# Performance work log

Hardware: AMD Instinct MI355X
Metric: run time of the kernel (lower is better)

The kernel has to match this reference:

```python
import jax, jax.numpy as jnp
import numpy as np

B, C, N, K = 2, 64, 20000, 16
COUT = 64


def setup_inputs() -> dict:
    key = jax.random.key(0)
    k1, k2, k3, k4, k5 = jax.random.split(key, 5)
    x = jax.random.normal(k1, (B, C, N, 1), dtype=jnp.float32)
    edge_index = jax.random.randint(k2, (2, B, N, K), 0, N)
    pos = jax.random.normal(k3, (B, 3, N, 1), dtype=jnp.float32)
    # BasicConv([2C, COUT]) -> 1x1 Conv2d weight [COUT, 2C] (+bias), then ReLU
    W = jax.random.normal(k4, (COUT, 2 * C), dtype=jnp.float32) * (1.0 / np.sqrt(2 * C))
    b = jax.random.normal(k5, (COUT,), dtype=jnp.float32) * 0.01
    return {"x": x, "edge_index": edge_index, "pos": pos, "W": W, "b": b}


def _gather(t, idx):
    # t: [B, C, N, 1], idx: [B, N, K] -> [B, C, N, K]
    t3 = t[..., 0]  # [B, C, N]
    return jax.vmap(lambda tb, ib: tb[:, ib])(t3, idx)


def reference(x, edge_index, pos, W, b):
    x_i = _gather(x, edge_index[1])           # [B, C, N, K] center
    x_j = _gather(x, edge_index[0])           # [B, C, N, K] neighbor
    feat = jnp.concatenate([x_i, x_j - x_i], axis=1)  # [B, 2C, N, K]
    # 1x1 conv + bias + ReLU
    out = jnp.einsum('oc,bcnk->bonk', W, feat) + b[None, :, None, None]
    out = jax.nn.relu(out)
    # distance-based suppression
    pos_i = _gather(pos, edge_index[1])       # [B, 3, N, K]
    pos_j = _gather(pos, edge_index[0])
    dis = jnp.sqrt(jnp.sum(jnp.square(pos_j - pos_i), axis=1))  # [B, N, K]
    suppression = 2.0 * jax.nn.sigmoid(-dis)[:, None, :, :]     # [B, 1, N, K]
    out = out * suppression
    max_value = jnp.max(out, axis=-1, keepdims=True)             # [B, COUT, N, 1]
    return max_value
```

## Files before the change

### kernel.cpp

```cpp
#include <hip/hip_runtime.h>
#include <math.h>

#define B_    2
#define C_    64
#define N_    20000
#define K_    16
#define COUT_ 64
#define TN1   64
#define NB1   ((N_ + TN1 - 1) / TN1)
#define TN2   16
#define NB2   (N_ / TN2)

typedef unsigned int   u32;
typedef unsigned short u16;

static __device__ __forceinline__ u16 f2bf(float f) {
    union { float f; u32 u; } v; v.f = f;
    u32 r = (v.u + 0x7FFFu + ((v.u >> 16) & 1u)) >> 16;
    return (u16)r;
}
static __device__ __forceinline__ float uasf(u32 u) {
    union { u32 u; float f; } v; v.u = u; return v.f;
}

__global__ __launch_bounds__(256)
void stage1(const float* __restrict__ x, const float* __restrict__ W,
            const float* __restrict__ bias,
            u16* __restrict__ zbuf, u16* __restrict__ ybuf) {
    __shared__ float xt[64][68];
    __shared__ float wc[64][130];

    const int bi   = blockIdx.x;
    const int b    = bi / NB1;
    const int n0   = (bi % NB1) * TN1;
    const int t    = threadIdx.x;
    const int lane = t & 63;
    const int w    = t >> 6;

    #pragma unroll
    for (int r = 0; r < 16; ++r) {
        int flat = r * 256 + t;
        int o = flat >> 6, c = flat & 63;
        float w1 = W[o * 128 + c];
        float w2 = W[o * 128 + 64 + c];
        wc[c][2 * o]     = w1 - w2;
        wc[c][2 * o + 1] = w2;
    }
    const float* xb = x + (size_t)b * C_ * N_;
    #pragma unroll
    for (int r = 0; r < 4; ++r) {
        int flat = r * 256 + t;
        int c = flat >> 4, ng = (flat & 15) * 4;
        int n = n0 + ng;
        float4 v;
        if (n + 3 < N_) {
            v = *(const float4*)&xb[c * N_ + n];
        } else {
            v.x = (n     < N_) ? xb[c * N_ + n    ] : 0.0f;
            v.y = (n + 1 < N_) ? xb[c * N_ + n + 1] : 0.0f;
            v.z = (n + 2 < N_) ? xb[c * N_ + n + 2] : 0.0f;
            v.w = (n + 3 < N_) ? xb[c * N_ + n + 3] : 0.0f;
        }
        *(float4*)&xt[c][ng] = v;
    }
    const float bo = bias[lane];
    __syncthreads();

    const int nb = w * 16;
    float4 z0 = {bo,bo,bo,bo}, z1 = z0, z2 = z0, z3 = z0;
    float4 y0 = {0,0,0,0},     y1 = y0, y2 = y0, y3 = y0;

#define FMA4(ZR, YR, XV) \
    ZR.x = fmaf(wv.x, XV.x, ZR.x);  YR.x = fmaf(wv.y, XV.x, YR.x); \
    ZR.y = fmaf(wv.x, XV.y, ZR.y);  YR.y = fmaf(wv.y, XV.y, YR.y); \
    ZR.z = fmaf(wv.x, XV.z, ZR.z);  YR.z = fmaf(wv.y, XV.z, YR.z); \
    ZR.w = fmaf(wv.x, XV.w, ZR.w);  YR.w = fmaf(wv.y, XV.w, YR.w);

    #pragma unroll 2
    for (int c = 0; c < 64; ++c) {
        float2 wv = *(const float2*)&wc[c][2 * lane];
        float4 xa = *(const float4*)&xt[c][nb];
        float4 xv1 = *(const float4*)&xt[c][nb + 4];
        float4 xv2 = *(const float4*)&xt[c][nb + 8];
        float4 xv3 = *(const float4*)&xt[c][nb + 12];
        FMA4(z0, y0, xa)
        FMA4(z1, y1, xv1)
        FMA4(z2, y2, xv2)
        FMA4(z3, y3, xv3)
    }
#undef FMA4

    {
        const size_t rowb = (size_t)b * N_;
        auto st = [&](int i, float zv, float yv) {
            int n = n0 + nb + i;
            if (n < N_) {
                size_t off = (rowb + n) * 64 + lane;
                zbuf[off] = f2bf(zv);
                ybuf[off] = f2bf(yv);
            }
        };
        st(0,  z0.x, y0.x); st(1,  z0.y, y0.y); st(2,  z0.z, y0.z); st(3,  z0.w, y0.w);
        st(4,  z1.x, y1.x); st(5,  z1.y, y1.y); st(6,  z1.z, y1.z); st(7,  z1.w, y1.w);
        st(8,  z2.x, y2.x); st(9,  z2.y, y2.y); st(10, z2.z, y2.z); st(11, z2.w, y2.w);
        st(12, z3.x, y3.x); st(13, z3.y, y3.y); st(14, z3.z, y3.z); st(15, z3.w, y3.w);
    }
}

__global__ __launch_bounds__(256)
void stage2(const int* __restrict__ ei, const float* __restrict__ pos,
            const u16* __restrict__ zbuf, const u16* __restrict__ ybuf,
            float* __restrict__ out) {
    __shared__ uint2 esl[TN2][17];
    __shared__ float tile[TN2][66];

    const int bi   = blockIdx.x;
    const int b    = bi / NB2;
    const int n0   = (bi % NB2) * TN2;
    const int t    = threadIdx.x;
    const int nl   = t >> 4;
    const int kh   = (t >> 3) & 1;
    const int cq   = t & 7;

    {
        const int    idx = n0 * K_ + t;
        const int*   e0  = ei + (size_t)b * N_ * K_;
        const int*   e1  = ei + ((size_t)B_ + b) * N_ * K_;
        const float* pb  = pos + (size_t)b * 3 * N_;
        int i0 = e0[idx], i1 = e1[idx];
        float dx = pb[i0]          - pb[i1];
        float dy = pb[N_ + i0]     - pb[N_ + i1];
        float dz = pb[2 * N_ + i0] - pb[2 * N_ + i1];
        float dis = sqrtf(dx * dx + dy * dy + dz * dz);
        float s = 2.0f / (1.0f + __expf(dis));
        esl[t >> 4][t & 15] = make_uint2((u32)i0 | ((u32)i1 << 16),
                                         __float_as_uint(s));
    }
    __syncthreads();

    const u16* zb = zbuf + (size_t)b * N_ * 64;
    const u16* yb = ybuf + (size_t)b * N_ * 64;

    float4 ma = {0,0,0,0}, mb = {0,0,0,0};

#define COMB(ZW, YW, MLO, MHI) { \
    float zl = uasf((ZW) << 16), zh = uasf((ZW) & 0xFFFF0000u); \
    float yl = uasf((YW) << 16), yh = uasf((YW) & 0xFFFF0000u); \
    MLO = fmaxf(MLO, fmaxf(zl + yl, 0.0f) * s); \
    MHI = fmaxf(MHI, fmaxf(zh + yh, 0.0f) * s); }

    #pragma unroll
    for (int i = 0; i < 8; ++i) {
        int   k = 2 * i + kh;
        uint2 e = esl[nl][k];
        int   i0 = (int)(e.x & 0xFFFFu);
        int   i1 = (int)(e.x >> 16);
        float s  = uasf(e.y);
        uint4 z4 = *((const uint4*)(zb + ((size_t)i1 << 6)) + cq);
        uint4 y4 = *((const uint4*)(yb + ((size_t)i0 << 6)) + cq);
        COMB(z4.x, y4.x, ma.x, ma.y)
        COMB(z4.y, y4.y, ma.z, ma.w)
        COMB(z4.z, y4.z, mb.x, mb.y)
        COMB(z4.w, y4.w, mb.z, mb.w)
    }
#undef COMB

    ma.x = fmaxf(ma.x, __shfl_xor(ma.x, 8));
    ma.y = fmaxf(ma.y, __shfl_xor(ma.y, 8));
    ma.z = fmaxf(ma.z, __shfl_xor(ma.z, 8));
    ma.w = fmaxf(ma.w, __shfl_xor(ma.w, 8));
    mb.x = fmaxf(mb.x, __shfl_xor(mb.x, 8));
    mb.y = fmaxf(mb.y, __shfl_xor(mb.y, 8));
    mb.z = fmaxf(mb.z, __shfl_xor(mb.z, 8));
    mb.w = fmaxf(mb.w, __shfl_xor(mb.w, 8));

    if (kh == 0) {
        int cb = cq * 8;
        *(float2*)&tile[nl][cb]     = make_float2(ma.x, ma.y);
        *(float2*)&tile[nl][cb + 2] = make_float2(ma.z, ma.w);
        *(float2*)&tile[nl][cb + 4] = make_float2(mb.x, mb.y);
        *(float2*)&tile[nl][cb + 6] = make_float2(mb.z, mb.w);
    }
    __syncthreads();

    #pragma unroll
    for (int r = 0; r < 4; ++r) {
        int flat = r * 256 + t;
        int o = flat >> 4, n2 = flat & 15;
        __builtin_nontemporal_store(tile[n2][o],
            &out[((size_t)b * COUT_ + o) * N_ + n0 + n2]);
    }
}

extern "C" void kernel_launch(void* const* d_in, const int* in_sizes, int n_in,
                              void* d_out, int out_size, void* d_ws, size_t ws_size,
                              hipStream_t stream) {
    const float* x    = (const float*)d_in[0];
    const int*   ei   = (const int*)  d_in[1];
    const float* pos  = (const float*)d_in[2];
    const float* W    = (const float*)d_in[3];
    const float* bias = (const float*)d_in[4];
    float*       out  = (float*)d_out;

    const size_t tabElems = (size_t)B_ * N_ * 64;
    u16* zbuf = (u16*)d_ws;
    u16* ybuf = zbuf + tabElems;

    hipLaunchKernelGGL(stage1, dim3(B_ * NB1), dim3(256), 0, stream,
                       x, W, bias, zbuf, ybuf);
    hipLaunchKernelGGL(stage2, dim3(B_ * NB2), dim3(256), 0, stream,
                       ei, pos, zbuf, ybuf, out);
}
```

Measured before the change: 107.9 us.

## Gather bf16 edge features into LDS and run per-edge conv with MFMA

```diff
diff --git a/kernel.cpp b/kernel.cpp
--- a/kernel.cpp
+++ b/kernel.cpp
@@ -6,13 +6,15 @@
 #define N_    20000
 #define K_    16
 #define COUT_ 64
-#define TN1   64
-#define NB1   ((N_ + TN1 - 1) / TN1)
-#define TN2   16
-#define NB2   (N_ / TN2)
+#define TNC   64
+#define NBC   ((N_ + TNC - 1) / TNC)
+#define TN    16
+#define NB    (N_ / TN)
 
 typedef unsigned int   u32;
 typedef unsigned short u16;
+typedef __attribute__((ext_vector_type(8))) short bf16x8;
+typedef __attribute__((ext_vector_type(4))) float f32x4;
 
 static __device__ __forceinline__ u16 f2bf(float f) {
     union { float f; u32 u; } v; v.f = f;
@@ -22,31 +24,43 @@
 static __device__ __forceinline__ float uasf(u32 u) {
     union { u32 u; float f; } v; v.u = u; return v.f;
 }
+static __device__ __forceinline__ u32 bfsub2(u32 bv, u32 av) {
+    float bl = uasf(bv << 16), bh = uasf(bv & 0xFFFF0000u);
+    float al = uasf(av << 16), ah = uasf(av & 0xFFFF0000u);
+    return (u32)f2bf(bl - al) | ((u32)f2bf(bh - ah) << 16);
+}
+
+#define SWZ(row, off) ((off) ^ (((row) & 7) << 4))
 
 __global__ __launch_bounds__(256)
-void stage1(const float* __restrict__ x, const float* __restrict__ W,
-            const float* __restrict__ bias,
-            u16* __restrict__ zbuf, u16* __restrict__ ybuf) {
-    __shared__ float xt[64][68];
-    __shared__ float wc[64][130];
-
-    const int bi   = blockIdx.x;
-    const int b    = bi / NB1;
-    const int n0   = (bi % NB1) * TN1;
-    const int t    = threadIdx.x;
-    const int lane = t & 63;
-    const int w    = t >> 6;
-
-    #pragma unroll
-    for (int r = 0; r < 16; ++r) {
-        int flat = r * 256 + t;
-        int o = flat >> 6, c = flat & 63;
-        float w1 = W[o * 128 + c];
-        float w2 = W[o * 128 + 64 + c];
-        wc[c][2 * o]     = w1 - w2;
-        wc[c][2 * o + 1] = w2;
-    }
-    const float* xb = x + (size_t)b * C_ * N_;
+void precast(const float* __restrict__ x, const float* __restrict__ W,
+             u16* __restrict__ xb, u16* __restrict__ wfrag) {
+    const int bi = blockIdx.x;
+    const int t  = threadIdx.x;
+
+    if (bi == B_ * NBC) {
+        const int l  = t & 63;
+        const int ot = t >> 6;
+        const int ro = (ot * 16 + (l & 15)) * 128 + ((l >> 4) << 3);
+        #pragma unroll
+        for (int ks = 0; ks < 4; ++ks) {
+            u32 p[4];
+            #pragma unroll
+            for (int jj = 0; jj < 4; ++jj) {
+                float v0 = W[ro + ks * 32 + 2 * jj];
+                float v1 = W[ro + ks * 32 + 2 * jj + 1];
+                p[jj] = (u32)f2bf(v0) | ((u32)f2bf(v1) << 16);
+            }
+            *(uint4*)&wfrag[(size_t)((ot * 4 + ks) * 64 + l) * 8] =
+                make_uint4(p[0], p[1], p[2], p[3]);
+        }
+        return;
+    }
+
+    __shared__ float tile[64][68];
+    const int b  = bi / NBC;
+    const int n0 = (bi % NBC) * TNC;
+    const float* xbase = x + (size_t)b * C_ * N_;
     #pragma unroll
     for (int r = 0; r < 4; ++r) {
         int flat = r * 256 + t;
@@ -54,132 +68,141 @@
         int n = n0 + ng;
         float4 v;
         if (n + 3 < N_) {
-            v = *(const float4*)&xb[c * N_ + n];
+            v = *(const float4*)&xbase[c * N_ + n];
         } else {
-            v.x = (n     < N_) ? xb[c * N_ + n    ] : 0.0f;
-            v.y = (n + 1 < N_) ? xb[c * N_ + n + 1] : 0.0f;
-            v.z = (n + 2 < N_) ? xb[c * N_ + n + 2] : 0.0f;
-            v.w = (n + 3 < N_) ? xb[c * N_ + n + 3] : 0.0f;
-        }
-        *(float4*)&xt[c][ng] = v;
-    }
-    const float bo = bias[lane];
-    __syncthreads();
-
-    const int nb = w * 16;
-    float4 z0 = {bo,bo,bo,bo}, z1 = z0, z2 = z0, z3 = z0;
-    float4 y0 = {0,0,0,0},     y1 = y0, y2 = y0, y3 = y0;
-
-#define FMA4(ZR, YR, XV) \
-    ZR.x = fmaf(wv.x, XV.x, ZR.x);  YR.x = fmaf(wv.y, XV.x, YR.x); \
-    ZR.y = fmaf(wv.x, XV.y, ZR.y);  YR.y = fmaf(wv.y, XV.y, YR.y); \
-    ZR.z = fmaf(wv.x, XV.z, ZR.z);  YR.z = fmaf(wv.y, XV.z, YR.z); \
-    ZR.w = fmaf(wv.x, XV.w, ZR.w);  YR.w = fmaf(wv.y, XV.w, YR.w);
-
-    #pragma unroll 2
-    for (int c = 0; c < 64; ++c) {
-        float2 wv = *(const float2*)&wc[c][2 * lane];
-        float4 xa = *(const float4*)&xt[c][nb];
-        float4 xv1 = *(const float4*)&xt[c][nb + 4];
-        float4 xv2 = *(const float4*)&xt[c][nb + 8];
-        float4 xv3 = *(const float4*)&xt[c][nb + 12];
-        FMA4(z0, y0, xa)
-        FMA4(z1, y1, xv1)
-        FMA4(z2, y2, xv2)
-        FMA4(z3, y3, xv3)
-    }
-#undef FMA4
+            v.x = (n     < N_) ? xbase[c * N_ + n    ] : 0.0f;
+            v.y = (n + 1 < N_) ? xbase[c * N_ + n + 1] : 0.0f;
+            v.z = (n + 2 < N_) ? xbase[c * N_ + n + 2] : 0.0f;
+            v.w = (n + 3 < N_) ? xbase[c * N_ + n + 3] : 0.0f;
+        }
+        *(float4*)&tile[c][ng] = v;
+    }
+    __syncthreads();
+
+    const int n = t >> 2, q = t & 3;
+    if (n0 + n < N_) {
+        u32 p[8];
+        #pragma unroll
+        for (int jj = 0; jj < 8; ++jj) {
+            float v0 = tile[q * 16 + 2 * jj][n];
+            float v1 = tile[q * 16 + 2 * jj + 1][n];
+            p[jj] = (u32)f2bf(v0) | ((u32)f2bf(v1) << 16);
+        }
+        u16* dst = xb + ((size_t)(b * N_ + n0 + n)) * 64 + q * 16;
+        *(uint4*)dst       = make_uint4(p[0], p[1], p[2], p[3]);
+        *(uint4*)(dst + 8) = make_uint4(p[4], p[5], p[6], p[7]);
+    }
+}
+
+__global__ __launch_bounds__(256)
+void fused(const int* __restrict__ ei, const float* __restrict__ pos,
+           const u16* __restrict__ xb, const u16* __restrict__ wfrag,
+           const float* __restrict__ bias, float* __restrict__ out) {
+    __shared__ u16   feat[256 * 128];
+    __shared__ uint2 esl[256];
+    __shared__ float otile[16][66];
+
+    const int bi   = blockIdx.x;
+    const int b    = bi / NB;
+    const int n0   = (bi % NB) * TN;
+    const int t    = threadIdx.x;
+    const int lane = t & 63;
+    const int w    = t >> 6;
+    const int g    = lane >> 4;
 
     {
-        const size_t rowb = (size_t)b * N_;
-        auto st = [&](int i, float zv, float yv) {
-            int n = n0 + nb + i;
-            if (n < N_) {
-                size_t off = (rowb + n) * 64 + lane;
-                zbuf[off] = f2bf(zv);
-                ybuf[off] = f2bf(yv);
-            }
-        };
-        st(0,  z0.x, y0.x); st(1,  z0.y, y0.y); st(2,  z0.z, y0.z); st(3,  z0.w, y0.w);
-        st(4,  z1.x, y1.x); st(5,  z1.y, y1.y); st(6,  z1.z, y1.z); st(7,  z1.w, y1.w);
-        st(8,  z2.x, y2.x); st(9,  z2.y, y2.y); st(10, z2.z, y2.z); st(11, z2.w, y2.w);
-        st(12, z3.x, y3.x); st(13, z3.y, y3.y); st(14, z3.z, y3.z); st(15, z3.w, y3.w);
-    }
-}
-
-__global__ __launch_bounds__(256)
-void stage2(const int* __restrict__ ei, const float* __restrict__ pos,
-            const u16* __restrict__ zbuf, const u16* __restrict__ ybuf,
-            float* __restrict__ out) {
-    __shared__ uint2 esl[TN2][17];
-    __shared__ float tile[TN2][66];
-
-    const int bi   = blockIdx.x;
-    const int b    = bi / NB2;
-    const int n0   = (bi % NB2) * TN2;
-    const int t    = threadIdx.x;
-    const int nl   = t >> 4;
-    const int kh   = (t >> 3) & 1;
-    const int cq   = t & 7;
-
-    {
-        const int    idx = n0 * K_ + t;
-        const int*   e0  = ei + (size_t)b * N_ * K_;
-        const int*   e1  = ei + ((size_t)B_ + b) * N_ * K_;
-        const float* pb  = pos + (size_t)b * 3 * N_;
-        int i0 = e0[idx], i1 = e1[idx];
+        const int idx = n0 * K_ + t;
+        int i0 = ei[(size_t)b * N_ * K_ + idx];
+        int i1 = ei[((size_t)B_ + b) * N_ * K_ + idx];
+        const float* pb = pos + (size_t)b * 3 * N_;
         float dx = pb[i0]          - pb[i1];
         float dy = pb[N_ + i0]     - pb[N_ + i1];
         float dz = pb[2 * N_ + i0] - pb[2 * N_ + i1];
         float dis = sqrtf(dx * dx + dy * dy + dz * dz);
         float s = 2.0f / (1.0f + __expf(dis));
-        esl[t >> 4][t & 15] = make_uint2((u32)i0 | ((u32)i1 << 16),
-                                         __float_as_uint(s));
-    }
-    __syncthreads();
-
-    const u16* zb = zbuf + (size_t)b * N_ * 64;
-    const u16* yb = ybuf + (size_t)b * N_ * 64;
-
-    float4 ma = {0,0,0,0}, mb = {0,0,0,0};
-
-#define COMB(ZW, YW, MLO, MHI) { \
-    float zl = uasf((ZW) << 16), zh = uasf((ZW) & 0xFFFF0000u); \
-    float yl = uasf((YW) << 16), yh = uasf((YW) & 0xFFFF0000u); \
-    MLO = fmaxf(MLO, fmaxf(zl + yl, 0.0f) * s); \
-    MHI = fmaxf(MHI, fmaxf(zh + yh, 0.0f) * s); }
-
-    #pragma unroll
-    for (int i = 0; i < 8; ++i) {
-        int   k = 2 * i + kh;
-        uint2 e = esl[nl][k];
-        int   i0 = (int)(e.x & 0xFFFFu);
-        int   i1 = (int)(e.x >> 16);
-        float s  = uasf(e.y);
-        uint4 z4 = *((const uint4*)(zb + ((size_t)i1 << 6)) + cq);
-        uint4 y4 = *((const uint4*)(yb + ((size_t)i0 << 6)) + cq);
-        COMB(z4.x, y4.x, ma.x, ma.y)
-        COMB(z4.y, y4.y, ma.z, ma.w)
-        COMB(z4.z, y4.z, mb.x, mb.y)
-        COMB(z4.w, y4.w, mb.z, mb.w)
-    }
-#undef COMB
-
-    ma.x = fmaxf(ma.x, __shfl_xor(ma.x, 8));
-    ma.y = fmaxf(ma.y, __shfl_xor(ma.y, 8));
-    ma.z = fmaxf(ma.z, __shfl_xor(ma.z, 8));
-    ma.w = fmaxf(ma.w, __shfl_xor(ma.w, 8));
-    mb.x = fmaxf(mb.x, __shfl_xor(mb.x, 8));
-    mb.y = fmaxf(mb.y, __shfl_xor(mb.y, 8));
-    mb.z = fmaxf(mb.z, __shfl_xor(mb.z, 8));
-    mb.w = fmaxf(mb.w, __shfl_xor(mb.w, 8));
-
-    if (kh == 0) {
-        int cb = cq * 8;
-        *(float2*)&tile[nl][cb]     = make_float2(ma.x, ma.y);
-        *(float2*)&tile[nl][cb + 2] = make_float2(ma.z, ma.w);
-        *(float2*)&tile[nl][cb + 4] = make_float2(mb.x, mb.y);
-        *(float2*)&tile[nl][cb + 6] = make_float2(mb.z, mb.w);
+        esl[t] = make_uint2((u32)i0 | ((u32)i1 << 16), __float_as_uint(s));
+    }
+    __syncthreads();
+
+    {
+        const uint4* xrow = (const uint4*)(xb + (size_t)b * N_ * 64);
+        const int cq = t & 7;
+        char* fb = (char*)feat;
+        #pragma unroll
+        for (int p = 0; p < 8; ++p) {
+            int e = p * 32 + (t >> 3);
+            uint2 ee = esl[e];
+            int i0 = (int)(ee.x & 0xFFFFu);
+            int i1 = (int)(ee.x >> 16);
+            uint4 a  = xrow[((size_t)i1 << 3) + cq];
+            uint4 bv = xrow[((size_t)i0 << 3) + cq];
+            *(uint4*)(fb + SWZ(e, e * 256 + cq * 16)) = a;
+            uint4 d;
+            d.x = bfsub2(bv.x, a.x);
+            d.y = bfsub2(bv.y, a.y);
+            d.z = bfsub2(bv.z, a.z);
+            d.w = bfsub2(bv.w, a.w);
+            *(uint4*)(fb + SWZ(e, e * 256 + 128 + cq * 16)) = d;
+        }
+    }
+
+    bf16x8 wf[16];
+    #pragma unroll
+    for (int f = 0; f < 16; ++f)
+        wf[f] = *(const bf16x8*)&wfrag[(size_t)(f * 64 + lane) * 8];
+
+    const int col = lane & 15;
+    const float bo0 = bias[col], bo1 = bias[16 + col],
+                bo2 = bias[32 + col], bo3 = bias[48 + col];
+    __syncthreads();
+
+    const char* fb = (const char*)feat;
+    #pragma unroll
+    for (int it = 0; it < 4; ++it) {
+        const int et  = it * 4 + w;
+        const int row = et * 16 + col;
+        const int rb  = row * 256 + g * 16;
+        bf16x8 a0 = *(const bf16x8*)(fb + SWZ(row, rb));
+        bf16x8 a1 = *(const bf16x8*)(fb + SWZ(row, rb + 64));
+        bf16x8 a2 = *(const bf16x8*)(fb + SWZ(row, rb + 128));
+        bf16x8 a3 = *(const bf16x8*)(fb + SWZ(row, rb + 192));
+        f32x4 ac0 = {0,0,0,0}, ac1 = ac0, ac2 = ac0, ac3 = ac0;
+        ac0 = __builtin_amdgcn_mfma_f32_16x16x32_bf16(a0, wf[0],  ac0, 0,0,0);
+        ac0 = __builtin_amdgcn_mfma_f32_16x16x32_bf16(a1, wf[1],  ac0, 0,0,0);
+        ac0 = __builtin_amdgcn_mfma_f32_16x16x32_bf16(a2, wf[2],  ac0, 0,0,0);
+        ac0 = __builtin_amdgcn_mfma_f32_16x16x32_bf16(a3, wf[3],  ac0, 0,0,0);
+        ac1 = __builtin_amdgcn_mfma_f32_16x16x32_bf16(a0, wf[4],  ac1, 0,0,0);
+        ac1 = __builtin_amdgcn_mfma_f32_16x16x32_bf16(a1, wf[5],  ac1, 0,0,0);
+        ac1 = __builtin_amdgcn_mfma_f32_16x16x32_bf16(a2, wf[6],  ac1, 0,0,0);
+        ac1 = __builtin_amdgcn_mfma_f32_16x16x32_bf16(a3, wf[7],  ac1, 0,0,0);
+        ac2 = __builtin_amdgcn_mfma_f32_16x16x32_bf16(a0, wf[8],  ac2, 0,0,0);
+        ac2 = __builtin_amdgcn_mfma_f32_16x16x32_bf16(a1, wf[9],  ac2, 0,0,0);
+        ac2 = __builtin_amdgcn_mfma_f32_16x16x32_bf16(a2, wf[10], ac2, 0,0,0);
+        ac2 = __builtin_amdgcn_mfma_f32_16x16x32_bf16(a3, wf[11], ac2, 0,0,0);
+        ac3 = __builtin_amdgcn_mfma_f32_16x16x32_bf16(a0, wf[12], ac3, 0,0,0);
+        ac3 = __builtin_amdgcn_mfma_f32_16x16x32_bf16(a1, wf[13], ac3, 0,0,0);
+        ac3 = __builtin_amdgcn_mfma_f32_16x16x32_bf16(a2, wf[14], ac3, 0,0,0);
+        ac3 = __builtin_amdgcn_mfma_f32_16x16x32_bf16(a3, wf[15], ac3, 0,0,0);
+
+        float m0 = 0.f, m1 = 0.f, m2 = 0.f, m3 = 0.f;
+#define EPI(REG) { \
+        float sv = uasf(esl[et * 16 + g * 4 + REG].y); \
+        m0 = fmaxf(m0, fmaxf(ac0[REG] + bo0, 0.f) * sv); \
+        m1 = fmaxf(m1, fmaxf(ac1[REG] + bo1, 0.f) * sv); \
+        m2 = fmaxf(m2, fmaxf(ac2[REG] + bo2, 0.f) * sv); \
+        m3 = fmaxf(m3, fmaxf(ac3[REG] + bo3, 0.f) * sv); }
+        EPI(0) EPI(1) EPI(2) EPI(3)
+#undef EPI
+        m0 = fmaxf(m0, __shfl_xor(m0, 16)); m0 = fmaxf(m0, __shfl_xor(m0, 32));
+        m1 = fmaxf(m1, __shfl_xor(m1, 16)); m1 = fmaxf(m1, __shfl_xor(m1, 32));
+        m2 = fmaxf(m2, __shfl_xor(m2, 16)); m2 = fmaxf(m2, __shfl_xor(m2, 32));
+        m3 = fmaxf(m3, __shfl_xor(m3, 16)); m3 = fmaxf(m3, __shfl_xor(m3, 32));
+        if (lane < 16) {
+            otile[et][col]      = m0;
+            otile[et][16 + col] = m1;
+            otile[et][32 + col] = m2;
+            otile[et][48 + col] = m3;
+        }
     }
     __syncthreads();
 
@@ -187,7 +210,7 @@
     for (int r = 0; r < 4; ++r) {
         int flat = r * 256 + t;
         int o = flat >> 4, n2 = flat & 15;
-        __builtin_nontemporal_store(tile[n2][o],
+        __builtin_nontemporal_store(otile[n2][o],
             &out[((size_t)b * COUT_ + o) * N_ + n0 + n2]);
     }
 }
@@ -202,12 +225,11 @@
     const float* bias = (const float*)d_in[4];
     float*       out  = (float*)d_out;
 
-    const size_t tabElems = (size_t)B_ * N_ * 64;
-    u16* zbuf = (u16*)d_ws;
-    u16* ybuf = zbuf + tabElems;
-
-    hipLaunchKernelGGL(stage1, dim3(B_ * NB1), dim3(256), 0, stream,
-                       x, W, bias, zbuf, ybuf);
-    hipLaunchKernelGGL(stage2, dim3(B_ * NB2), dim3(256), 0, stream,
-                       ei, pos, zbuf, ybuf, out);
-}
+    u16* xb    = (u16*)d_ws;
+    u16* wfrag = xb + (size_t)B_ * N_ * 64;
+
+    hipLaunchKernelGGL(precast, dim3(B_ * NBC + 1), dim3(256), 0, stream,
+                       x, W, xb, wfrag);
+    hipLaunchKernelGGL(fused, dim3(B_ * NB), dim3(256), 0, stream,
+                       ei, pos, xb, wfrag, bias, out);
+}
```

Measured after the change: 113.0 us. 1.05x slower.
